# Optimization experiments

Hardware: AMD Instinct MI355X
Metric: run time of the kernel (lower is better)

The kernel has to match this reference:

```python
import jax, jax.numpy as jnp
import numpy as np

B, S, HID = 2, 1024, 4096
NH, NKV, HD = 32, 8, 128
GROUPS = NH // NKV  # 4
BITS = 8
SCALING = HD ** -0.5


def quantize_lastdim(x, bits=BITS):
    """Asymmetric min-max fake-quant per row of the last dim (groupsize=-1),
    matching ActQuantizer.find_params + quantize/dequantize."""
    qmax = float(2 ** bits - 1)
    xmin = jnp.minimum(jnp.min(x, axis=-1, keepdims=True), 0.0)
    xmax = jnp.maximum(jnp.max(x, axis=-1, keepdims=True), 0.0)
    rng = xmax - xmin
    scale = jnp.where(rng == 0, 1.0, rng / qmax)
    zero = jnp.round(-xmin / scale)
    q = jnp.clip(jnp.round(x / scale) + zero, 0.0, qmax)
    return (q - zero) * scale


def rotate_half(x):
    x1, x2 = jnp.split(x, 2, axis=-1)
    return jnp.concatenate([-x2, x1], axis=-1)


def setup_inputs() -> dict:
    key = jax.random.key(0)
    ks = jax.random.split(key, 5)
    hidden_states = jax.random.normal(ks[0], (B, S, HID), dtype=jnp.float32)
    w_std = 0.02
    Wq = w_std * jax.random.normal(ks[1], (NH * HD, HID), dtype=jnp.float32)
    Wk = w_std * jax.random.normal(ks[2], (NKV * HD, HID), dtype=jnp.float32)
    Wv = w_std * jax.random.normal(ks[3], (NKV * HD, HID), dtype=jnp.float32)
    Wo = w_std * jax.random.normal(ks[4], (HID, NH * HD), dtype=jnp.float32)
    # RoPE tables (theta=10000)
    inv_freq = 1.0 / (10000.0 ** (jnp.arange(0, HD, 2, dtype=jnp.float32) / HD))
    freqs = jnp.outer(jnp.arange(S, dtype=jnp.float32), inv_freq)  # [S, HD/2]
    emb = jnp.concatenate([freqs, freqs], axis=-1)  # [S, HD]
    cos = jnp.broadcast_to(jnp.cos(emb)[None], (B, S, HD)).astype(jnp.float32)
    sin = jnp.broadcast_to(jnp.sin(emb)[None], (B, S, HD)).astype(jnp.float32)
    # additive causal mask [B,1,S,S]
    causal = jnp.tril(jnp.ones((S, S), dtype=bool))
    attention_mask = jnp.where(causal, 0.0, -1e9).astype(jnp.float32)
    attention_mask = jnp.broadcast_to(attention_mask[None, None], (B, 1, S, S))
    return {"hidden_states": hidden_states, "cos": cos, "sin": sin,
            "attention_mask": attention_mask, "Wq": Wq, "Wk": Wk, "Wv": Wv, "Wo": Wo}


def reference(hidden_states, cos, sin, attention_mask, Wq, Wk, Wv, Wo):
    b, s, _ = hidden_states.shape
    # projections -> [B, H, S, D]
    q = (hidden_states @ Wq.T).reshape(b, s, NH, HD).transpose(0, 2, 1, 3)
    k = (hidden_states @ Wk.T).reshape(b, s, NKV, HD).transpose(0, 2, 1, 3)
    v = (hidden_states @ Wv.T).reshape(b, s, NKV, HD).transpose(0, 2, 1, 3)
    # RoPE (HF: unsqueeze cos/sin at head dim)
    c = cos[:, None, :, :]
    si = sin[:, None, :, :]
    q = q * c + rotate_half(q) * si
    k = k * c + rotate_half(k) * si
    # SmoothK per-channel: subtract per-channel mean over the sequence
    # (softmax-invariant outlier smoothing of K before quantization)
    k = k - jnp.mean(k, axis=2, keepdims=True)
    # activation fake-quant of Q, K (per token over head_dim)
    q = quantize_lastdim(q)
    k = quantize_lastdim(k)
    # V quantized along the sequence axis (module transposes dims 2,3 first)
    v = quantize_lastdim(v.transpose(0, 1, 3, 2)).transpose(0, 1, 3, 2)
    # GQA repeat
    k_rep = jnp.repeat(k, GROUPS, axis=1)
    v_rep = jnp.repeat(v, GROUPS, axis=1)
    scores = jnp.einsum('bhqd,bhkd->bhqk', q, k_rep) * SCALING + attention_mask
    w = jax.nn.softmax(scores.astype(jnp.float32), axis=-1).astype(q.dtype)
    # fake-quant attention weights per row (groupsize=-1, so no padding)
    w = quantize_lastdim(w)
    attn = jnp.einsum('bhqk,bhkd->bhqd', w, v_rep)
    attn = attn.transpose(0, 2, 1, 3).reshape(b, s, NH * HD)
    out = attn @ Wo.T
    return (out, w)
```

## Files before the change

### kernel.cpp

```cpp
#include <hip/hip_runtime.h>
#include <math.h>
#include <stdint.h>

typedef unsigned int u32;
typedef unsigned short u16;
typedef __bf16 bf16x8 __attribute__((ext_vector_type(8)));
typedef float f32x4 __attribute__((ext_vector_type(4)));
typedef unsigned short u16x8 __attribute__((ext_vector_type(8)));
typedef unsigned short u16x4 __attribute__((ext_vector_type(4)));

constexpr int   Bb  = 2;
constexpr int   Ss  = 1024;
constexpr int   HID = 4096;
constexpr int   NH  = 32;
constexpr int   NKV = 8;
constexpr int   HD  = 128;
constexpr float SCALING = 0.0883883476483184405501f;

enum { M_QKV = 0, M_OUT = 3 };

__device__ __forceinline__ u16 f2bf(float f) {
  u32 u = __builtin_bit_cast(u32, f);
  u = u + 0x7fffu + ((u >> 16) & 1u);
  return (u16)(u >> 16);
}

__device__ __forceinline__ void gld_lds16(const void* g, void* l) {
  __builtin_amdgcn_global_load_lds(
      (const __attribute__((address_space(1))) u32*)(uintptr_t)g,
      (__attribute__((address_space(3))) u32*)(uintptr_t)l, 16, 0, 0);
}

template <int MODE>
__global__ __launch_bounds__(256, 2) void mfma_gemm(
    const u16* __restrict__ Abf_g,
    const u16* __restrict__ B0, const u16* __restrict__ B1,
    const u16* __restrict__ B2,
    u16* __restrict__ Cq, float* __restrict__ Ckf, float* __restrict__ Cv,
    float* __restrict__ Cfo,
    const float* __restrict__ cosp, const float* __restrict__ sinp,
    int K) {
  __shared__ u16 As[3][128 * 32];
  __shared__ u16 Bs[3][256 * 32];

  const int tid = threadIdx.x;
  const int lane = tid & 63;
  const int wid = tid >> 6;
  const int wr = wid >> 1;
  const int wc = wid & 1;
  const int fr = lane & 15;
  const int fq = lane >> 4;

  const int bx = blockIdx.x;
  const int m0 = blockIdx.y * 128;
  int nloc = 0;

  const u16* Abf = Abf_g + (size_t)m0 * K;
  const u16* Bp = nullptr;
  int which = 0;

  if (MODE == M_QKV) {
    if (bx < 16)      { which = 0; Bp = B0 + (size_t)bx * 256 * K;        nloc = bx * 256; }
    else if (bx < 20) { which = 1; Bp = B1 + (size_t)(bx - 16) * 256 * K; nloc = (bx - 16) * 256; }
    else              { which = 2; Bp = B2 + (size_t)(bx - 20) * 256 * K; nloc = (bx - 20) * 256; }
  } else {
    Bp = B0 + (size_t)bx * 256 * K;
    nloc = bx * 256;
  }

  f32x4 acc[4][8];
#pragma unroll
  for (int i = 0; i < 4; i++)
#pragma unroll
    for (int j = 0; j < 8; j++) acc[i][j] = (f32x4){0.f, 0.f, 0.f, 0.f};

  const int prow = wid * 16 + (lane >> 2);
  const int psl = lane & 3;

  auto stA = [&](int t, int s, int e) {
    const int row = e * 64 + prow;
    gld_lds16(Abf + (size_t)row * K + t * 32 + ((psl ^ ((row >> 1) & 3)) * 8),
              &As[s][(e * 64 + wid * 16) * 32]);
  };
  auto stB = [&](int t, int s, int e) {
    const int row = e * 64 + prow;
    gld_lds16(Bp + (size_t)row * K + t * 32 + ((psl ^ ((row >> 1) & 3)) * 8),
              &Bs[s][(e * 64 + wid * 16) * 32]);
  };

  const int nk = K >> 5;

  stA(0, 0, 0); stA(0, 0, 1);
  stB(0, 0, 0); stB(0, 0, 1); stB(0, 0, 2); stB(0, 0, 3);
  stA(1, 1, 0); stA(1, 1, 1);
  stB(1, 1, 0); stB(1, 1, 1); stB(1, 1, 2); stB(1, 1, 3);
  asm volatile("s_waitcnt vmcnt(6)" ::: "memory");
  __builtin_amdgcn_sched_barrier(0);
  __builtin_amdgcn_s_barrier();

  int buf = 0, nxt = 2;
  for (int kt = 0; kt < nk; ++kt) {
    const bool st = (kt + 2 < nk);
    bf16x8 av[4], bv[4];

#pragma unroll
    for (int i = 0; i < 4; ++i) {
      const int r = wr * 64 + i * 16 + fr;
      av[i] = *(const bf16x8*)&As[buf][r * 32 + ((fq ^ ((r >> 1) & 3)) * 8)];
    }
#pragma unroll
    for (int j = 0; j < 4; ++j) {
      const int r = wc * 128 + j * 16 + fr;
      bv[j] = *(const bf16x8*)&Bs[buf][r * 32 + ((fq ^ ((r >> 1) & 3)) * 8)];
    }
    if (st) { stA(kt + 2, nxt, 0); stA(kt + 2, nxt, 1); stB(kt + 2, nxt, 0); }
    __builtin_amdgcn_s_barrier();
    asm volatile("s_waitcnt lgkmcnt(0)" ::: "memory");
    __builtin_amdgcn_sched_barrier(0);
    __builtin_amdgcn_s_setprio(1);
#pragma unroll
    for (int i = 0; i < 4; i++)
#pragma unroll
      for (int j = 0; j < 4; j++)
        acc[i][j] = __builtin_amdgcn_mfma_f32_16x16x32_bf16(av[i], bv[j], acc[i][j], 0, 0, 0);
    __builtin_amdgcn_s_setprio(0);

#pragma unroll
    for (int j = 0; j < 4; ++j) {
      const int r = wc * 128 + (j + 4) * 16 + fr;
      bv[j] = *(const bf16x8*)&Bs[buf][r * 32 + ((fq ^ ((r >> 1) & 3)) * 8)];
    }
    if (st) { stB(kt + 2, nxt, 1); stB(kt + 2, nxt, 2); stB(kt + 2, nxt, 3); }
    __builtin_amdgcn_s_barrier();
    asm volatile("s_waitcnt lgkmcnt(0)" ::: "memory");
    __builtin_amdgcn_sched_barrier(0);
    __builtin_amdgcn_s_setprio(1);
#pragma unroll
    for (int i = 0; i < 4; i++)
#pragma unroll
      for (int j = 0; j < 4; j++)
        acc[i][j + 4] = __builtin_amdgcn_mfma_f32_16x16x32_bf16(av[i], bv[j], acc[i][j + 4], 0, 0, 0);
    __builtin_amdgcn_s_setprio(0);

    if (st) {
      asm volatile("s_waitcnt vmcnt(6)" ::: "memory");
    } else {
      asm volatile("s_waitcnt vmcnt(0)" ::: "memory");
    }
    __builtin_amdgcn_sched_barrier(0);
    __builtin_amdgcn_s_barrier();
    buf = (buf == 2) ? 0 : buf + 1;
    nxt = (nxt == 2) ? 0 : nxt + 1;
  }

  if (MODE == M_QKV && which <= 1) {
#pragma unroll
    for (int i = 0; i < 4; i++) {
#pragma unroll
      for (int e = 0; e < 4; e++) {
        const int m = m0 + wr * 64 + i * 16 + fq * 4 + e;
        const int b = m >> 10, s = m & 1023;
        const float* cp = cosp + ((size_t)b * Ss + s) * HD;
        const float* sp2 = sinp + ((size_t)b * Ss + s) * HD;
        float r[8];
#pragma unroll
        for (int j = 0; j < 4; j++) {
          const float c = cp[j * 16 + fr];
          const float sv = sp2[j * 16 + fr];
          const float x1 = acc[i][j][e], x2 = acc[i][j + 4][e];
          r[j] = x1 * c - x2 * sv;
          r[j + 4] = x2 * c + x1 * sv;
        }
        if (which == 0) {
          float mn = 0.f, mx = 0.f;
#pragma unroll
          for (int j = 0; j < 8; j++) { mn = fminf(mn, r[j]); mx = fmaxf(mx, r[j]); }
#pragma unroll
          for (int o = 1; o < 16; o <<= 1) {
            mn = fminf(mn, __shfl_xor(mn, o));
            mx = fmaxf(mx, __shfl_xor(mx, o));
          }
          const float rng = mx - mn;
          const float scale = (rng == 0.f) ? 1.f : rng / 255.f;
          const float zero = rintf(-mn / scale);
          const int hq = bx * 2 + wc;
          u16* qp = Cq + ((size_t)(b * NH + hq) * Ss + s) * HD + fr;
#pragma unroll
          for (int j = 0; j < 8; j++) {
            const float qv = fminf(fmaxf(rintf(r[j] / scale) + zero, 0.f), 255.f);
            qp[j * 16] = f2bf((qv - zero) * scale);
          }
        } else {
          const int kh = (bx - 16) * 2 + wc;
          float* kp = Ckf + ((size_t)(b * NKV + kh) * Ss + s) * HD + fr;
#pragma unroll
          for (int j = 0; j < 8; j++) kp[j * 16] = r[j];
        }
      }
    }
  } else {
#pragma unroll
    for (int i = 0; i < 4; i++) {
#pragma unroll
      for (int j = 0; j < 8; j++) {
        const int n = nloc + wc * 128 + j * 16 + fr;
        const int mb = m0 + wr * 64 + i * 16 + fq * 4;
        if (MODE == M_QKV) {
          const int b = mb >> 10, s = mb & 1023, h = n >> 7, d = n & 127;
          float4 v4 = {acc[i][j][0], acc[i][j][1], acc[i][j][2], acc[i][j][3]};
          *(float4*)&Cv[((size_t)(b * NKV + h) * HD + d) * Ss + s] = v4;
        } else {
#pragma unroll
          for (int e = 0; e < 4; e++)
            Cfo[(size_t)(mb + e) * HID + n] = acc[i][j][e];
        }
      }
    }
  }
}

__global__ __launch_bounds__(256) void fused_attn(
    const u16* __restrict__ qb,
    const u16* __restrict__ kb,
    const u16* __restrict__ vTb,
    float* __restrict__ wout,
    u16* __restrict__ attnb) {
  __shared__ u16 Ks[2][64 * 128];
  __shared__ u16 Vs[2][128 * 64];
  __shared__ u16 plds[4][16 * 64];
  __shared__ float scl_l[4][16];

  const int a = 15 - (int)(blockIdx.x >> 6);
  const int bh = blockIdx.x & 63;
  const int b = bh >> 5, h = bh & 31;
  const int kv = h >> 2;
  const int tid = threadIdx.x;
  const int lane = tid & 63;
  const int wq = tid >> 6;
  const int fr = lane & 15, fq = lane >> 4;

  const int nt = a + 1;
  const int Q0 = a * 64;
  const int qw0 = Q0 + wq * 16;

  const u16* Kb = kb + (size_t)(b * NKV + kv) * Ss * HD;
  const u16* Vb = vTb + (size_t)(b * NKV + kv) * HD * Ss;
  float* wrow = wout + (size_t)bh * Ss * Ss;

  auto stageK = [&](int t, int s) {
#pragma unroll
    for (int c = 0; c < 4; ++c) {
      const int idx0 = (c * 4 + wq) * 64;
      const int idx = idx0 + lane;
      const int row = idx >> 4, sl = idx & 15;
      const int slot = sl ^ (row & 15);
      gld_lds16(Kb + (size_t)(t * 64 + row) * HD + slot * 8, &Ks[s][idx0 * 8]);
    }
  };
  auto stageV = [&](int t, int s) {
#pragma unroll
    for (int c = 0; c < 4; ++c) {
      const int idx0 = (c * 4 + wq) * 64;
      const int idx = idx0 + lane;
      const int d = idx >> 3, sl = idx & 7;
      const int slot = sl ^ (d & 7);
      gld_lds16(Vb + (size_t)d * Ss + t * 64 + slot * 8, &Vs[s][idx0 * 8]);
    }
  };

  stageK(0, 0);

  if (a < 15) {
    const int base = 64 * nt;
    const int n4 = 16 * (15 - a);
#pragma unroll
    for (int r0 = 0; r0 < 4; ++r0) {
      const int row = Q0 + r0 * 16 + (tid >> 4);
      float4* wp = (float4*)&wrow[(size_t)row * Ss + base];
      for (int c = tid & 15; c < n4; c += 16) wp[c] = float4{0.f, 0.f, 0.f, 0.f};
    }
  }

  bf16x8 qf[4];
#pragma unroll
  for (int kk = 0; kk < 4; kk++)
    qf[kk] = *(const bf16x8*)&qb[((size_t)bh * Ss + qw0 + fr) * HD + kk * 32 + fq * 8];

  float m[4], l[4];
#pragma unroll
  for (int i = 0; i < 4; i++) { m[i] = -1e30f; l[i] = 0.f; }

  for (int t = 0; t < nt; ++t) {
    if (t + 1 < nt) {
      stageK(t + 1, (t + 1) & 1);
      asm volatile("s_waitcnt vmcnt(4)" ::: "memory");
    } else {
      asm volatile("s_waitcnt vmcnt(0)" ::: "memory");
    }
    __builtin_amdgcn_sched_barrier(0);
    __builtin_amdgcn_s_barrier();
    const u16* Kt = &Ks[t & 1][0];

    f32x4 sa[4];
#pragma unroll
    for (int jn = 0; jn < 4; jn++) sa[jn] = (f32x4){0.f, 0.f, 0.f, 0.f};
#pragma unroll
    for (int kk = 0; kk < 4; ++kk) {
      bf16x8 kfv[4];
#pragma unroll
      for (int jn = 0; jn < 4; ++jn) {
        const int row = jn * 16 + fr;
        kfv[jn] = *(const bf16x8*)&Kt[row * 128 + (((kk * 4 + fq) ^ fr) * 8)];
      }
#pragma unroll
      for (int jn = 0; jn < 4; ++jn)
        sa[jn] = __builtin_amdgcn_mfma_f32_16x16x32_bf16(qf[kk], kfv[jn], sa[jn], 0, 0, 0);
    }

    const bool diag = (t == a);
#pragma unroll
    for (int e = 0; e < 4; ++e) {
      const int qrow = qw0 + fq * 4 + e;
      float sv[4];
      float rmax = -1e30f;
#pragma unroll
      for (int jn = 0; jn < 4; ++jn) {
        float s = sa[jn][e] * SCALING;
        if (diag && (t * 64 + jn * 16 + fr > qrow)) s = -1e30f;
        sv[jn] = s;
        rmax = fmaxf(rmax, s);
      }
#pragma unroll
      for (int o = 1; o < 16; o <<= 1) rmax = fmaxf(rmax, __shfl_xor(rmax, o));
      const float mn = fmaxf(m[e], rmax);
      const float cc = __expf(m[e] - mn);
      float rs = __expf(sv[0] - mn) + __expf(sv[1] - mn) +
                 __expf(sv[2] - mn) + __expf(sv[3] - mn);
#pragma unroll
      for (int o = 1; o < 16; o <<= 1) rs += __shfl_xor(rs, o);
      l[e] = l[e] * cc + rs;
      m[e] = mn;
    }
    __builtin_amdgcn_s_barrier();
  }

  float scl[4];
#pragma unroll
  for (int e = 0; e < 4; e++) scl[e] = 1.f / (255.f * l[e]);
  if (fr == 0) {
#pragma unroll
    for (int e = 0; e < 4; e++) scl_l[wq][fq * 4 + e] = scl[e];
  }

  f32x4 acc2[8];
#pragma unroll
  for (int j = 0; j < 8; j++) acc2[j] = (f32x4){0.f, 0.f, 0.f, 0.f};

  u16* pl = &plds[wq][0];
  const int wrrow = lane >> 2, wrq = lane & 3;
  const float sclr = scl_l[wq][wrrow];

  stageK(0, 0);
  stageV(0, 0);
  for (int t = 0; t < nt; ++t) {
    if (t + 1 < nt) {
      stageK(t + 1, (t + 1) & 1);
      stageV(t + 1, (t + 1) & 1);
      asm volatile("s_waitcnt vmcnt(8)" ::: "memory");
    } else {
      asm volatile("s_waitcnt vmcnt(0)" ::: "memory");
    }
    __builtin_amdgcn_sched_barrier(0);
    __builtin_amdgcn_s_barrier();
    const u16* Kt = &Ks[t & 1][0];
    const u16* Vt = &Vs[t & 1][0];

    f32x4 sa[4];
#pragma unroll
    for (int jn = 0; jn < 4; jn++) sa[jn] = (f32x4){0.f, 0.f, 0.f, 0.f};
#pragma unroll
    for (int kk = 0; kk < 4; ++kk) {
      bf16x8 kfv[4];
#pragma unroll
      for (int jn = 0; jn < 4; ++jn) {
        const int row = jn * 16 + fr;
        kfv[jn] = *(const bf16x8*)&Kt[row * 128 + (((kk * 4 + fq) ^ fr) * 8)];
      }
#pragma unroll
      for (int jn = 0; jn < 4; ++jn)
        sa[jn] = __builtin_amdgcn_mfma_f32_16x16x32_bf16(qf[kk], kfv[jn], sa[jn], 0, 0, 0);
    }

    const bool diag = (t == a);
#pragma unroll
    for (int e = 0; e < 4; ++e) {
      const int qrow = qw0 + fq * 4 + e;
      const int r16 = fq * 4 + e;
#pragma unroll
      for (int jn = 0; jn < 4; ++jn) {
        const int kc = t * 64 + jn * 16 + fr;
        float qv = 0.f;
        if (!diag || kc <= qrow)
          qv = rintf(fminf(255.f * __expf(sa[jn][e] * SCALING - m[e]), 255.f));
        const int col = jn * 16 + fr;
        const int byte = r16 * 128 + (((col >> 3) ^ (r16 & 7)) * 16) + (col & 7) * 2;
        *(u16*)((char*)pl + byte) = f2bf(qv);
      }
    }

    {
      const int s0 = (2 * wrq) ^ (wrrow & 7);
      const int s1 = (2 * wrq + 1) ^ (wrrow & 7);
      bf16x8 p0 = *(const bf16x8*)((char*)pl + wrrow * 128 + s0 * 16);
      bf16x8 p1 = *(const bf16x8*)((char*)pl + wrrow * 128 + s1 * 16);
      float* wp = &wrow[(size_t)(qw0 + wrrow) * Ss + t * 64 + wrq * 16];
      float4 o0, o1, o2, o3;
      o0.x = (float)p0[0] * sclr; o0.y = (float)p0[1] * sclr;
      o0.z = (float)p0[2] * sclr; o0.w = (float)p0[3] * sclr;
      o1.x = (float)p0[4] * sclr; o1.y = (float)p0[5] * sclr;
      o1.z = (float)p0[6] * sclr; o1.w = (float)p0[7] * sclr;
      o2.x = (float)p1[0] * sclr; o2.y = (float)p1[1] * sclr;
      o2.z = (float)p1[2] * sclr; o2.w = (float)p1[3] * sclr;
      o3.x = (float)p1[4] * sclr; o3.y = (float)p1[5] * sclr;
      o3.z = (float)p1[6] * sclr; o3.w = (float)p1[7] * sclr;
      ((float4*)wp)[0] = o0; ((float4*)wp)[1] = o1;
      ((float4*)wp)[2] = o2; ((float4*)wp)[3] = o3;
    }

#pragma unroll
    for (int kk2 = 0; kk2 < 2; ++kk2) {
      const bf16x8 pa = *(const bf16x8*)((char*)pl + fr * 128 + (((kk2 * 4 + fq) ^ (fr & 7)) * 16));
#pragma unroll
      for (int jn2 = 0; jn2 < 8; ++jn2) {
        const int d = jn2 * 16 + fr;
        const bf16x8 vb = *(const bf16x8*)&Vt[d * 64 + (((kk2 * 4 + fq) ^ (d & 7)) * 8)];
        acc2[jn2] = __builtin_amdgcn_mfma_f32_16x16x32_bf16(pa, vb, acc2[jn2], 0, 0, 0);
      }
    }
    __builtin_amdgcn_s_barrier();
  }

#pragma unroll
  for (int e = 0; e < 4; ++e) {
    const int qrow = qw0 + fq * 4 + e;
#pragma unroll
    for (int jn2 = 0; jn2 < 8; ++jn2)
      attnb[((size_t)b * Ss + qrow) * HID + h * HD + jn2 * 16 + fr] =
          f2bf(acc2[jn2][e] * scl[e]);
  }
}

constexpr int CB_HS = Bb * Ss * HID / 2048;
constexpr int CB_WQ = NH * HD * HID / 2048;
constexpr int CB_WK = NKV * HD * HID / 2048;
constexpr int CB_WV = CB_WK;
constexpr int CB_WO = HID * NH * HD / 2048;

__global__ __launch_bounds__(256) void convert_all(
    const float* __restrict__ hs, const float* __restrict__ wq,
    const float* __restrict__ wk, const float* __restrict__ wv,
    const float* __restrict__ wo,
    u16* __restrict__ hsb, u16* __restrict__ wqb, u16* __restrict__ wkb,
    u16* __restrict__ wvb, u16* __restrict__ wob) {
  const int bid = blockIdx.x;
  const float* src;
  u16* dst;
  int base;
  if (bid < CB_HS) { src = hs; dst = hsb; base = 0; }
  else if (bid < CB_HS + CB_WQ) { src = wq; dst = wqb; base = CB_HS; }
  else if (bid < CB_HS + CB_WQ + CB_WK) { src = wk; dst = wkb; base = CB_HS + CB_WQ; }
  else if (bid < CB_HS + CB_WQ + CB_WK + CB_WV) { src = wv; dst = wvb; base = CB_HS + CB_WQ + CB_WK; }
  else { src = wo; dst = wob; base = CB_HS + CB_WQ + CB_WK + CB_WV; }
  const int i = (bid - base) * 256 + threadIdx.x;
  float4 a = ((const float4*)src)[2 * i];
  float4 b = ((const float4*)src)[2 * i + 1];
  u16x8 t;
  t[0] = f2bf(a.x); t[1] = f2bf(a.y); t[2] = f2bf(a.z); t[3] = f2bf(a.w);
  t[4] = f2bf(b.x); t[5] = f2bf(b.y); t[6] = f2bf(b.z); t[7] = f2bf(b.w);
  ((u16x8*)dst)[i] = t;
}

__global__ __launch_bounds__(256) void vquant(const float* __restrict__ vT,
                                              u16* __restrict__ vTb) {
  const float* p = vT + (size_t)blockIdx.x * Ss;
  const int t = threadIdx.x;
  float4 x = ((const float4*)p)[t];
  float mn = fminf(0.f, fminf(fminf(x.x, x.y), fminf(x.z, x.w)));
  float mx = fmaxf(0.f, fmaxf(fmaxf(x.x, x.y), fmaxf(x.z, x.w)));
#pragma unroll
  for (int o = 32; o; o >>= 1) {
    mn = fminf(mn, __shfl_xor(mn, o));
    mx = fmaxf(mx, __shfl_xor(mx, o));
  }
  __shared__ float smn[4], smx[4];
  const int wid = t >> 6, lane = t & 63;
  if (lane == 0) { smn[wid] = mn; smx[wid] = mx; }
  __syncthreads();
  mn = fminf(fminf(smn[0], smn[1]), fminf(smn[2], smn[3]));
  mx = fmaxf(fmaxf(smx[0], smx[1]), fmaxf(smx[2], smx[3]));
  float rng = mx - mn;
  float scale = (rng == 0.f) ? 1.f : rng / 255.f;
  float zero = rintf(-mn / scale);
  u16x4 o4;
  o4[0] = f2bf((fminf(fmaxf(rintf(x.x / scale) + zero, 0.f), 255.f) - zero) * scale);
  o4[1] = f2bf((fminf(fmaxf(rintf(x.y / scale) + zero, 0.f), 255.f) - zero) * scale);
  o4[2] = f2bf((fminf(fmaxf(rintf(x.z / scale) + zero, 0.f), 255.f) - zero) * scale);
  o4[3] = f2bf((fminf(fmaxf(rintf(x.w / scale) + zero, 0.f), 255.f) - zero) * scale);
  ((u16x4*)vTb)[(size_t)blockIdx.x * 256 + t] = o4;
}

__global__ __launch_bounds__(1024) void kmean_kernel(const float* __restrict__ k,
                                                     float* __restrict__ kmean) {
  const int bh = blockIdx.x;
  const int d = threadIdx.x & 127;
  const int sl = threadIdx.x >> 7;
  const float* p = k + (size_t)bh * Ss * HD;
  float sum = 0.f;
  for (int s = sl; s < Ss; s += 8) sum += p[(size_t)s * HD + d];
  __shared__ float lds[8][128];
  lds[sl][d] = sum;
  __syncthreads();
  if (threadIdx.x < 128) {
    float t = 0.f;
#pragma unroll
    for (int i = 0; i < 8; i++) t += lds[i][threadIdx.x];
    kmean[bh * HD + threadIdx.x] = t * (1.f / 1024.f);
  }
}

__global__ __launch_bounds__(256) void k_subquant(const float* __restrict__ k,
                                                  u16* __restrict__ kb,
                                                  const float* __restrict__ kmean) {
  const int row = blockIdx.x * 4 + (threadIdx.x >> 6);
  const int lane = threadIdx.x & 63;
  const int bh = row >> 10;
  const float* p = k + (size_t)row * HD;
  float x1 = p[lane] - kmean[bh * HD + lane];
  float x2 = p[lane + 64] - kmean[bh * HD + lane + 64];
  float mn = fminf(0.f, fminf(x1, x2));
  float mx = fmaxf(0.f, fmaxf(x1, x2));
#pragma unroll
  for (int o = 32; o; o >>= 1) {
    mn = fminf(mn, __shfl_xor(mn, o));
    mx = fmaxf(mx, __shfl_xor(mx, o));
  }
  float rng = mx - mn;
  float scale = (rng == 0.f) ? 1.f : rng / 255.f;
  float zero = rintf(-mn / scale);
  float q1 = fminf(fmaxf(rintf(x1 / scale) + zero, 0.f), 255.f);
  float q2 = fminf(fmaxf(rintf(x2 / scale) + zero, 0.f), 255.f);
  kb[(size_t)row * HD + lane] = f2bf((q1 - zero) * scale);
  kb[(size_t)row * HD + lane + 64] = f2bf((q2 - zero) * scale);
}

extern "C" void kernel_launch(void* const* d_in, const int* in_sizes, int n_in,
                              void* d_out, int out_size, void* d_ws, size_t ws_size,
                              hipStream_t stream) {
  const float* hs = (const float*)d_in[0];
  const float* cosp = (const float*)d_in[1];
  const float* sinp = (const float*)d_in[2];
  const float* Wq = (const float*)d_in[4];
  const float* Wk = (const float*)d_in[5];
  const float* Wv = (const float*)d_in[6];
  const float* Wo = (const float*)d_in[7];

  float* out = (float*)d_out;
  float* wout = out + (size_t)Bb * Ss * HID;

  char* wsp = (char*)d_ws;
  auto alloc = [&](size_t bytes) {
    char* p = wsp;
    wsp += (bytes + 255) & ~(size_t)255;
    return p;
  };
  float* k     = (float*)alloc((size_t)Bb * NKV * Ss * HD * 4);
  float* vT    = (float*)alloc((size_t)Bb * NKV * Ss * HD * 4);
  float* kmean = (float*)alloc((size_t)Bb * NKV * HD * 4);
  u16* hsb = (u16*)alloc((size_t)Bb * Ss * HID * 2);
  u16* qb  = (u16*)alloc((size_t)Bb * NH * Ss * HD * 2);
  u16* kb  = (u16*)alloc((size_t)Bb * NKV * Ss * HD * 2);
  u16* vTb = (u16*)alloc((size_t)Bb * NKV * Ss * HD * 2);
  u16* Wqb = (u16*)alloc((size_t)NH * HD * HID * 2);
  u16* Wkb = (u16*)alloc((size_t)NKV * HD * HID * 2);
  u16* Wvb = (u16*)alloc((size_t)NKV * HD * HID * 2);
  u16* Wob = (u16*)alloc((size_t)HID * NH * HD * 2);
  u16* attnb = (u16*)alloc((size_t)Bb * Ss * HID * 2);

  convert_all<<<CB_HS + CB_WQ + CB_WK + CB_WV + CB_WO, 256, 0, stream>>>(
      hs, Wq, Wk, Wv, Wo, hsb, Wqb, Wkb, Wvb, Wob);

  mfma_gemm<M_QKV><<<dim3(24, 16), 256, 0, stream>>>(
      hsb, Wqb, Wkb, Wvb, qb, k, vT, nullptr, cosp, sinp, HID);

  vquant<<<Bb * NKV * HD, 256, 0, stream>>>(vT, vTb);
  kmean_kernel<<<Bb * NKV, 1024, 0, stream>>>(k, kmean);
  k_subquant<<<(Bb * NKV * Ss) / 4, 256, 0, stream>>>(k, kb, kmean);

  fused_attn<<<dim3(1024), 256, 0, stream>>>(qb, kb, vTb, wout, attnb);

  mfma_gemm<M_OUT><<<dim3(16, 16), 256, 0, stream>>>(
      attnb, Wob, nullptr, nullptr, nullptr, nullptr, nullptr, out,
      nullptr, nullptr, HID);
}
```

Baseline: 419.7 us.

## Retile projection GEMMs to 256x128 tiles with 8 waves and K-step 64

The QKV and output projection GEMMs now use 512-thread blocks. Each block computes a 256x128 tile, and each wave owns 32 rows across the full 128 columns, so one head maps to one block. The K tile grows from 32 to 64 with an 8-way XOR swizzle, global pointers are precomputed, and K becomes a template parameter. The goal is to halve the number of barrier-synchronised K iterations and to match the tile to the head width. In exchange, LDS use per block rises to about 144 KB, which allows only one block per CU, and the grid is smaller (384 and 256 blocks).

```diff
diff --git a/kernel.cpp b/kernel.cpp
--- a/kernel.cpp
+++ b/kernel.cpp
@@ -31,112 +31,150 @@
       (__attribute__((address_space(3))) u32*)(uintptr_t)l, 16, 0, 0);
 }
 
-template <int MODE>
-__global__ __launch_bounds__(256, 2) void mfma_gemm(
+template <int MODE, int K>
+__global__ __launch_bounds__(512, 1) void mfma_gemm(
     const u16* __restrict__ Abf_g,
     const u16* __restrict__ B0, const u16* __restrict__ B1,
     const u16* __restrict__ B2,
     u16* __restrict__ Cq, float* __restrict__ Ckf, float* __restrict__ Cv,
     float* __restrict__ Cfo,
-    const float* __restrict__ cosp, const float* __restrict__ sinp,
-    int K) {
-  __shared__ u16 As[3][128 * 32];
-  __shared__ u16 Bs[3][256 * 32];
+    const float* __restrict__ cosp, const float* __restrict__ sinp) {
+  __shared__ u16 As[3][256 * 64];
+  __shared__ u16 Bs[3][128 * 64];
 
   const int tid = threadIdx.x;
   const int lane = tid & 63;
   const int wid = tid >> 6;
-  const int wr = wid >> 1;
-  const int wc = wid & 1;
   const int fr = lane & 15;
   const int fq = lane >> 4;
 
   const int bx = blockIdx.x;
-  const int m0 = blockIdx.y * 128;
-  int nloc = 0;
+  const int m0 = blockIdx.y * 256;
 
   const u16* Abf = Abf_g + (size_t)m0 * K;
   const u16* Bp = nullptr;
   int which = 0;
 
   if (MODE == M_QKV) {
-    if (bx < 16)      { which = 0; Bp = B0 + (size_t)bx * 256 * K;        nloc = bx * 256; }
-    else if (bx < 20) { which = 1; Bp = B1 + (size_t)(bx - 16) * 256 * K; nloc = (bx - 16) * 256; }
-    else              { which = 2; Bp = B2 + (size_t)(bx - 20) * 256 * K; nloc = (bx - 20) * 256; }
+    if (bx < 32)      { which = 0; Bp = B0 + (size_t)bx * 128 * K; }
+    else if (bx < 40) { which = 1; Bp = B1 + (size_t)(bx - 32) * 128 * K; }
+    else              { which = 2; Bp = B2 + (size_t)(bx - 40) * 128 * K; }
   } else {
-    Bp = B0 + (size_t)bx * 256 * K;
-    nloc = bx * 256;
-  }
-
-  f32x4 acc[4][8];
-#pragma unroll
-  for (int i = 0; i < 4; i++)
+    Bp = B0 + (size_t)bx * 128 * K;
+  }
+
+  f32x4 acc[2][8];
+#pragma unroll
+  for (int i = 0; i < 2; i++)
 #pragma unroll
     for (int j = 0; j < 8; j++) acc[i][j] = (f32x4){0.f, 0.f, 0.f, 0.f};
 
-  const int prow = wid * 16 + (lane >> 2);
-  const int psl = lane & 3;
-
-  auto stA = [&](int t, int s, int e) {
-    const int row = e * 64 + prow;
-    gld_lds16(Abf + (size_t)row * K + t * 32 + ((psl ^ ((row >> 1) & 3)) * 8),
-              &As[s][(e * 64 + wid * 16) * 32]);
+  const int srow8 = lane >> 3;
+  const int ssl = lane & 7;
+  const u16* gA[4];
+  const u16* gB[2];
+#pragma unroll
+  for (int p = 0; p < 4; ++p) {
+    const int row = p * 64 + wid * 8 + srow8;
+    gA[p] = Abf + (size_t)row * K + ((ssl ^ (row & 7)) * 8);
+  }
+#pragma unroll
+  for (int p = 0; p < 2; ++p) {
+    const int row = p * 64 + wid * 8 + srow8;
+    gB[p] = Bp + (size_t)row * K + ((ssl ^ (row & 7)) * 8);
+  }
+
+  auto stA = [&](int t, int s, int p) {
+    gld_lds16(gA[p] + t * 64, &As[s][(p * 64 + wid * 8) * 64]);
   };
-  auto stB = [&](int t, int s, int e) {
-    const int row = e * 64 + prow;
-    gld_lds16(Bp + (size_t)row * K + t * 32 + ((psl ^ ((row >> 1) & 3)) * 8),
-              &Bs[s][(e * 64 + wid * 16) * 32]);
+  auto stB = [&](int t, int s, int p) {
+    gld_lds16(gB[p] + t * 64, &Bs[s][(p * 64 + wid * 8) * 64]);
   };
 
-  const int nk = K >> 5;
-
-  stA(0, 0, 0); stA(0, 0, 1);
-  stB(0, 0, 0); stB(0, 0, 1); stB(0, 0, 2); stB(0, 0, 3);
-  stA(1, 1, 0); stA(1, 1, 1);
-  stB(1, 1, 0); stB(1, 1, 1); stB(1, 1, 2); stB(1, 1, 3);
+  auto rdA = [&](int s, int i, int ks) -> bf16x8 {
+    const int r = wid * 32 + i * 16 + fr;
+    return *(const bf16x8*)&As[s][r * 64 + (((ks * 4 + fq) ^ (r & 7)) * 8)];
+  };
+  auto rdB = [&](int s, int j, int ks) -> bf16x8 {
+    const int r = j * 16 + fr;
+    return *(const bf16x8*)&Bs[s][r * 64 + (((ks * 4 + fq) ^ (r & 7)) * 8)];
+  };
+
+  static_assert((K >> 6) == 64, "nk = 64 K-tiles of 64");
+  const int nk = K >> 6;
+
+#pragma unroll
+  for (int p = 0; p < 4; ++p) stA(0, 0, p);
+#pragma unroll
+  for (int p = 0; p < 2; ++p) stB(0, 0, p);
+#pragma unroll
+  for (int p = 0; p < 4; ++p) stA(1, 1, p);
+#pragma unroll
+  for (int p = 0; p < 2; ++p) stB(1, 1, p);
   asm volatile("s_waitcnt vmcnt(6)" ::: "memory");
   __builtin_amdgcn_sched_barrier(0);
   __builtin_amdgcn_s_barrier();
 
   int buf = 0, nxt = 2;
-  for (int kt = 0; kt < nk; ++kt) {
-    const bool st = (kt + 2 < nk);
-    bf16x8 av[4], bv[4];
-
-#pragma unroll
-    for (int i = 0; i < 4; ++i) {
-      const int r = wr * 64 + i * 16 + fr;
-      av[i] = *(const bf16x8*)&As[buf][r * 32 + ((fq ^ ((r >> 1) & 3)) * 8)];
-    }
-#pragma unroll
-    for (int j = 0; j < 4; ++j) {
-      const int r = wc * 128 + j * 16 + fr;
-      bv[j] = *(const bf16x8*)&Bs[buf][r * 32 + ((fq ^ ((r >> 1) & 3)) * 8)];
-    }
-    if (st) { stA(kt + 2, nxt, 0); stA(kt + 2, nxt, 1); stB(kt + 2, nxt, 0); }
+  for (int t = 0; t < nk; ++t) {
+    const bool st = (t + 2 < nk);
+    bf16x8 av[2], bv[4];
+
+    av[0] = rdA(buf, 0, 0); av[1] = rdA(buf, 1, 0);
+    bv[0] = rdB(buf, 0, 0); bv[1] = rdB(buf, 1, 0);
+    bv[2] = rdB(buf, 2, 0); bv[3] = rdB(buf, 3, 0);
+    if (st) { stA(t + 2, nxt, 0); stA(t + 2, nxt, 1); }
     __builtin_amdgcn_s_barrier();
     asm volatile("s_waitcnt lgkmcnt(0)" ::: "memory");
     __builtin_amdgcn_sched_barrier(0);
     __builtin_amdgcn_s_setprio(1);
 #pragma unroll
-    for (int i = 0; i < 4; i++)
+    for (int i = 0; i < 2; i++)
 #pragma unroll
       for (int j = 0; j < 4; j++)
         acc[i][j] = __builtin_amdgcn_mfma_f32_16x16x32_bf16(av[i], bv[j], acc[i][j], 0, 0, 0);
     __builtin_amdgcn_s_setprio(0);
-
-#pragma unroll
-    for (int j = 0; j < 4; ++j) {
-      const int r = wc * 128 + (j + 4) * 16 + fr;
-      bv[j] = *(const bf16x8*)&Bs[buf][r * 32 + ((fq ^ ((r >> 1) & 3)) * 8)];
-    }
-    if (st) { stB(kt + 2, nxt, 1); stB(kt + 2, nxt, 2); stB(kt + 2, nxt, 3); }
+    __builtin_amdgcn_s_barrier();
+
+    bv[0] = rdB(buf, 4, 0); bv[1] = rdB(buf, 5, 0);
+    bv[2] = rdB(buf, 6, 0); bv[3] = rdB(buf, 7, 0);
+    if (st) { stA(t + 2, nxt, 2); stA(t + 2, nxt, 3); }
     __builtin_amdgcn_s_barrier();
     asm volatile("s_waitcnt lgkmcnt(0)" ::: "memory");
     __builtin_amdgcn_sched_barrier(0);
     __builtin_amdgcn_s_setprio(1);
 #pragma unroll
-    for (int i = 0; i < 4; i++)
+    for (int i = 0; i < 2; i++)
+#pragma unroll
+      for (int j = 0; j < 4; j++)
+        acc[i][j + 4] = __builtin_amdgcn_mfma_f32_16x16x32_bf16(av[i], bv[j], acc[i][j + 4], 0, 0, 0);
+    __builtin_amdgcn_s_setprio(0);
+    __builtin_amdgcn_s_barrier();
+
+    av[0] = rdA(buf, 0, 1); av[1] = rdA(buf, 1, 1);
+    bv[0] = rdB(buf, 0, 1); bv[1] = rdB(buf, 1, 1);
+    bv[2] = rdB(buf, 2, 1); bv[3] = rdB(buf, 3, 1);
+    if (st) { stB(t + 2, nxt, 0); stB(t + 2, nxt, 1); }
+    __builtin_amdgcn_s_barrier();
+    asm volatile("s_waitcnt lgkmcnt(0)" ::: "memory");
+    __builtin_amdgcn_sched_barrier(0);
+    __builtin_amdgcn_s_setprio(1);
+#pragma unroll
+    for (int i = 0; i < 2; i++)
+#pragma unroll
+      for (int j = 0; j < 4; j++)
+        acc[i][j] = __builtin_amdgcn_mfma_f32_16x16x32_bf16(av[i], bv[j], acc[i][j], 0, 0, 0);
+    __builtin_amdgcn_s_setprio(0);
+    __builtin_amdgcn_s_barrier();
+
+    bv[0] = rdB(buf, 4, 1); bv[1] = rdB(buf, 5, 1);
+    bv[2] = rdB(buf, 6, 1); bv[3] = rdB(buf, 7, 1);
+    __builtin_amdgcn_s_barrier();
+    asm volatile("s_waitcnt lgkmcnt(0)" ::: "memory");
+    __builtin_amdgcn_sched_barrier(0);
+    __builtin_amdgcn_s_setprio(1);
+#pragma unroll
+    for (int i = 0; i < 2; i++)
 #pragma unroll
       for (int j = 0; j < 4; j++)
         acc[i][j + 4] = __builtin_amdgcn_mfma_f32_16x16x32_bf16(av[i], bv[j], acc[i][j + 4], 0, 0, 0);
@@ -155,10 +193,10 @@
 
   if (MODE == M_QKV && which <= 1) {
 #pragma unroll
-    for (int i = 0; i < 4; i++) {
+    for (int i = 0; i < 2; i++) {
 #pragma unroll
       for (int e = 0; e < 4; e++) {
-        const int m = m0 + wr * 64 + i * 16 + fq * 4 + e;
+        const int m = m0 + wid * 32 + i * 16 + fq * 4 + e;
         const int b = m >> 10, s = m & 1023;
         const float* cp = cosp + ((size_t)b * Ss + s) * HD;
         const float* sp2 = sinp + ((size_t)b * Ss + s) * HD;
@@ -183,7 +221,7 @@
           const float rng = mx - mn;
           const float scale = (rng == 0.f) ? 1.f : rng / 255.f;
           const float zero = rintf(-mn / scale);
-          const int hq = bx * 2 + wc;
+          const int hq = bx;
           u16* qp = Cq + ((size_t)(b * NH + hq) * Ss + s) * HD + fr;
 #pragma unroll
           for (int j = 0; j < 8; j++) {
@@ -191,7 +229,7 @@
             qp[j * 16] = f2bf((qv - zero) * scale);
           }
         } else {
-          const int kh = (bx - 16) * 2 + wc;
+          const int kh = bx - 32;
           float* kp = Ckf + ((size_t)(b * NKV + kh) * Ss + s) * HD + fr;
 #pragma unroll
           for (int j = 0; j < 8; j++) kp[j * 16] = r[j];
@@ -200,16 +238,17 @@
     }
   } else {
 #pragma unroll
-    for (int i = 0; i < 4; i++) {
+    for (int i = 0; i < 2; i++) {
 #pragma unroll
       for (int j = 0; j < 8; j++) {
-        const int n = nloc + wc * 128 + j * 16 + fr;
-        const int mb = m0 + wr * 64 + i * 16 + fq * 4;
+        const int mb = m0 + wid * 32 + i * 16 + fq * 4;
         if (MODE == M_QKV) {
-          const int b = mb >> 10, s = mb & 1023, h = n >> 7, d = n & 127;
+          const int b = mb >> 10, s = mb & 1023;
+          const int h = bx - 40, d = j * 16 + fr;
           float4 v4 = {acc[i][j][0], acc[i][j][1], acc[i][j][2], acc[i][j][3]};
           *(float4*)&Cv[((size_t)(b * NKV + h) * HD + d) * Ss + s] = v4;
         } else {
+          const int n = bx * 128 + j * 16 + fr;
 #pragma unroll
           for (int e = 0; e < 4; e++)
             Cfo[(size_t)(mb + e) * HID + n] = acc[i][j][e];
@@ -589,8 +628,8 @@
   convert_all<<<CB_HS + CB_WQ + CB_WK + CB_WV + CB_WO, 256, 0, stream>>>(
       hs, Wq, Wk, Wv, Wo, hsb, Wqb, Wkb, Wvb, Wob);
 
-  mfma_gemm<M_QKV><<<dim3(24, 16), 256, 0, stream>>>(
-      hsb, Wqb, Wkb, Wvb, qb, k, vT, nullptr, cosp, sinp, HID);
+  mfma_gemm<M_QKV, HID><<<dim3(48, 8), 512, 0, stream>>>(
+      hsb, Wqb, Wkb, Wvb, qb, k, vT, nullptr, cosp, sinp);
 
   vquant<<<Bb * NKV * HD, 256, 0, stream>>>(vT, vTb);
   kmean_kernel<<<Bb * NKV, 1024, 0, stream>>>(k, kmean);
@@ -598,7 +637,7 @@
 
   fused_attn<<<dim3(1024), 256, 0, stream>>>(qb, kb, vTb, wout, attnb);
 
-  mfma_gemm<M_OUT><<<dim3(16, 16), 256, 0, stream>>>(
+  mfma_gemm<M_OUT, HID><<<dim3(32, 8), 512, 0, stream>>>(
       attnb, Wob, nullptr, nullptr, nullptr, nullptr, nullptr, out,
-      nullptr, nullptr, HID);
-}
+      nullptr, nullptr);
+}
```

Result: slower. 428.2 us (+2.0%).
